# Kernel tuning notes

Hardware: AMD Instinct MI355X
Metric: run time of the kernel (lower is better)

The kernel has to match this reference:

```python
import jax, jax.numpy as jnp
import numpy as np
from jax import lax

# Module hyperparameters (match init_kwargs)
N_EXPERTS = 8
TOP_K = 2
N_CLUSTERS = 64
TEMP = 1.0
BETA = 0.9        # LIF membrane decay
VTH = 1.0         # LIF firing threshold
SURR_ALPHA = 4.0  # surrogate-gradient sharpness


@jax.custom_vjp
def spike(u):
    # Heaviside spike with sigmoid surrogate gradient (standard SNN practice)
    return (u >= 0).astype(u.dtype)

def _spike_fwd(u):
    return spike(u), u

def _spike_bwd(u, g):
    s = jax.nn.sigmoid(SURR_ALPHA * u)
    return (g * SURR_ALPHA * s * (1.0 - s),)

spike.defvjp(_spike_fwd, _spike_bwd)


def lif(x):
    """LIF neuron over leading time axis. x: (T, ...). Returns spikes (T, ...)."""
    def step(v, xt):
        v = BETA * v + xt
        s = spike(v - VTH)
        return v - s * VTH, s  # soft reset
    _, spikes = lax.scan(step, jnp.zeros_like(x[0]), x)
    return spikes


def setup_inputs() -> dict:
    key = jax.random.key(0)
    k1, k2, k3 = jax.random.split(key, 3)
    T, B, S, D = 4, 2, 1024, 1024
    ef = 4096 // N_EXPERTS  # 512
    x = jax.random.normal(k1, (T, B, S, D), dtype=jnp.float32)
    w_up = jax.random.normal(k2, (N_EXPERTS, D, ef), dtype=jnp.float32) / np.sqrt(D)
    w_down = jax.random.normal(k3, (N_EXPERTS, ef, D), dtype=jnp.float32) / np.sqrt(ef)
    expert_bias = jnp.zeros((N_EXPERTS,), dtype=jnp.float32)
    return {"x": x, "w_up": w_up, "w_down": w_down, "expert_bias": expert_bias}


def reference(x, w_up, w_down, expert_bias):
    T, B, S, D = x.shape
    N = B * S
    xf = x.reshape(T, N, D)

    # --- routing: LIF spikes -> cluster firing rates -> expert scores ---
    rs = lif(xf)                      # (T, N, D)
    fr = rs.mean(axis=0)              # (N, D) mean firing rate
    nc = N_CLUSTERS
    # feature d belongs to cluster d % nc -> reshape(N, D//nc, nc) sums same residues
    cr = fr.reshape(N, D // nc, nc).sum(axis=1) / (D // nc)       # (N, nc)
    cpe = nc // N_EXPERTS
    es = cr.reshape(N, N_EXPERTS, cpe).mean(axis=-1)              # (N, E)
    es = es / max(TEMP, 0.01) + expert_bias

    # --- top-k expert selection ---
    ts, ti = lax.top_k(es, TOP_K)                                 # (N, k)
    tw = jax.nn.softmax(ts, axis=-1).astype(x.dtype)              # (N, k)
    # combined per-(token, expert) weight: sum_k 1[ti==e] * tw
    w = (jax.nn.one_hot(ti, N_EXPERTS, dtype=x.dtype) * tw[..., None]).sum(axis=1)  # (N, E)

    # --- expert FFN with LIF nonlinearities (all experts, masked combine) ---
    # LIF is independent per (token, feature), so computing every expert on every
    # token and weighting by w (zero for unselected) matches the masked dispatch.
    h = jnp.einsum('tnd,edf->tenf', xf, w_up)                     # (T, E, N, ef)
    hs = lif(h)
    o = jnp.einsum('tenf,efd->tend', hs, w_down)                  # (T, E, N, D)
    os = lif(o)
    out = jnp.einsum('tend,ne->tnd', os, w).reshape(T, B, S, D)

    # --- load balance loss ---
    ef_frac = jax.nn.one_hot(ti, N_EXPERTS, dtype=jnp.float32).sum(axis=(0, 1)) / (N * TOP_K)
    rp = jax.nn.softmax(es, axis=-1).mean(axis=0)
    lb = N_EXPERTS * (ef_frac * rp).sum()
    return out, lb
```

## Files before the change

### kernel.cpp

```cpp
#include <hip/hip_runtime.h>
#include <cstdint>
#include <cstddef>

#define T_   4
#define NTOK 2048
#define D_   1024
#define EF   512
#define NE   8
#define TP   8

typedef __attribute__((ext_vector_type(4))) double d4;

#define WS_RP    0
#define WS_CNT   131072
#define WS_LTOK  131104
#define WS_LW    196640
#define WS_GMASK 327712

__global__ __launch_bounds__(256) void moe_routing(
    const float* __restrict__ x, const float* __restrict__ bias,
    double* __restrict__ rp, int* __restrict__ cnt,
    int* __restrict__ ltok, double* __restrict__ lw)
{
    const int n   = blockIdx.x;
    const int tid = threadIdx.x;
    __shared__ int scnt[NE];
    if (tid < NE) scnt[tid] = 0;
    __syncthreads();

    int c = 0;
#pragma unroll
    for (int j = 0; j < 4; ++j) {
        const int d = j * 256 + tid;
        double v = 0.0;
#pragma unroll
        for (int t = 0; t < T_; ++t) {
            v = 0.9 * v + (double)x[((size_t)t * NTOK + n) * D_ + d];
            if (v - 1.0 >= 0.0) { ++c; v -= 1.0; }
        }
    }
    c += __shfl_xor(c, 1);
    c += __shfl_xor(c, 2);
    c += __shfl_xor(c, 4);
    if ((tid & 7) == 0) atomicAdd(&scnt[(tid >> 3) & 7], c);
    __syncthreads();

    if (tid == 0) {
        double es[NE];
#pragma unroll
        for (int e = 0; e < NE; ++e)
            es[e] = (double)scnt[e] * (1.0 / 512.0) + (double)bias[e];

        int i0 = 0; double b0 = es[0];
        for (int e = 1; e < NE; ++e) if (es[e] > b0) { b0 = es[e]; i0 = e; }
        int i1 = -1; double b1 = -1e300;
        for (int e = 0; e < NE; ++e) if (e != i0 && es[e] > b1) { b1 = es[e]; i1 = e; }

        const double e1 = exp(b1 - b0);
        const double w0 = 1.0 / (1.0 + e1);
        const double w1 = e1 / (1.0 + e1);

        double mx = es[0];
        for (int e = 1; e < NE; ++e) mx = es[e] > mx ? es[e] : mx;
        double s = 0.0, ex[NE];
        for (int e = 0; e < NE; ++e) { ex[e] = exp(es[e] - mx); s += ex[e]; }
        for (int e = 0; e < NE; ++e) rp[(size_t)n * NE + e] = ex[e] / s;

        int s0 = atomicAdd(&cnt[i0], 1);
        ltok[i0 * NTOK + s0] = n; lw[i0 * NTOK + s0] = w0;
        int s1 = atomicAdd(&cnt[i1], 1);
        ltok[i1 * NTOK + s1] = n; lw[i1 * NTOK + s1] = w1;
    }
}

__global__ __launch_bounds__(256) void moe_finalize(
    const double* __restrict__ rp, const int* __restrict__ cnt,
    float* __restrict__ out_lb)
{
    __shared__ double red[256][NE];
    const int tid = threadIdx.x;
    double a[NE];
#pragma unroll
    for (int e = 0; e < NE; ++e) a[e] = 0.0;
    for (int n = tid; n < NTOK; n += 256)
#pragma unroll
        for (int e = 0; e < NE; ++e) a[e] += rp[(size_t)n * NE + e];
#pragma unroll
    for (int e = 0; e < NE; ++e) red[tid][e] = a[e];
    __syncthreads();
    if (tid < NE) {
        double s = 0.0;
        for (int i = 0; i < 256; ++i) s += red[i][tid];
        red[0][tid] = s;
    }
    __syncthreads();
    if (tid == 0) {
        double lb = 0.0;
#pragma unroll
        for (int e = 0; e < NE; ++e)
            lb += ((double)cnt[e] / (double)(NTOK * 2)) * (red[0][e] / (double)NTOK);
        out_lb[0] = (float)(8.0 * lb);
    }
}

__device__ __forceinline__ int dec_idx(double val, int* fam) {
    const double r0 = (val - 96.0) * 0.25;
    const int i0 = (int)r0;
    if ((double)i0 == r0 && i0 >= 0 && i0 < 16) { *fam = 0; return i0; }
    const double r1 = (val - 6.0) * 0.0625;
    const int i1 = (int)r1;
    if ((double)i1 == r1 && i1 >= 0 && i1 < 16) { *fam = 1; return i1; }
    *fam = -1; return 0;
}

struct Frag {
    int vA, kA, uB, kB;
    int vC[4], uC[4];
    int bad;
};

__device__ __forceinline__ Frag probe_layout(int l) {
    Frag fr; fr.bad = 0;
    const d4 zz = {0.0, 0.0, 0.0, 0.0};
    const double dl = (double)l;
    const d4 Dv = __builtin_amdgcn_mfma_f64_16x16x4f64(dl, 1.0, zz, 0, 0, 0);
    const d4 Du = __builtin_amdgcn_mfma_f64_16x16x4f64(1.0, dl, zz, 0, 0, 0);
    int famA = -1, famB = -1;
#pragma unroll
    for (int r = 0; r < 4; ++r) {
        int fa, fb;
        fr.vC[r] = dec_idx(Dv[r], &fa);
        fr.uC[r] = dec_idx(Du[r], &fb);
        if (r == 0) { famA = fa; famB = fb; }
        fr.bad |= (fa != famA) | (fb != famB) | (fa < 0) | (fb < 0);
    }
    fr.vA = (famA == 0) ? (l & 15) : (l >> 2);
    fr.kA = (famA == 0) ? (l >> 4) : (l & 3);
    fr.uB = (famB == 0) ? (l & 15) : (l >> 2);
    fr.kB = (famB == 0) ? (l >> 4) : (l & 3);
    const d4 D3 = __builtin_amdgcn_mfma_f64_16x16x4f64(
        (double)(1 << fr.kA), (double)(16 << fr.kB), zz, 0, 0, 0);
#pragma unroll
    for (int r = 0; r < 4; ++r) fr.bad |= (D3[r] != 1360.0);
    return fr;
}

__device__ __forceinline__ size_t gm_row(int e, int pairIdx, int t) {
    return ((size_t)((e << 11) + pairIdx) * 4 + t) * 32;
}

__global__ __launch_bounds__(256, 4) void moe_up(
    const float* __restrict__ x, const float* __restrict__ wup,
    const int* __restrict__ cnt, const int* __restrict__ ltok,
    unsigned short* __restrict__ gmask)
{
    const int gid  = blockIdx.x;
    const int e    = gid & 7;
    const int hf   = (gid >> 3) & 1;
    const int tile = gid >> 4;
    const int c    = cnt[e];
    const int base = tile * TP;
    if (base >= c) return;

    const int tid = threadIdx.x;
    const int w   = tid >> 6;
    const int l   = tid & 63;

    __shared__ int    s_tok[TP];
    __shared__ float  xs[32][132];
    __shared__ double dtile[4][16][17];
    __shared__ int s_bad;

    if (tid < TP) {
        const int idx = base + tid;
        s_tok[tid] = (idx < c) ? ltok[e * NTOK + idx] : ltok[e * NTOK + base];
    }
    if (tid == 0) s_bad = 0;
    __syncthreads();

    const Frag fr = probe_layout(l);
    if (fr.bad) atomicOr(&s_bad, 1);
    __syncthreads();

    if (s_bad) {
        unsigned short* gm16 = gmask;
        for (int i = tid; i < TP * 4 * 16; i += 256) {
            const int pr = i >> 6;
            gm16[gm_row(e, base + pr, (i >> 4) & 3) + hf * 16 + (i & 15)] = 0;
        }
        __syncthreads();
        for (int ci = tid; ci < TP * 256; ci += 256) {
            const int pair = ci >> 8;
            const int f    = hf * 256 + (ci & 255);
            const float* wc = wup + (size_t)e * D_ * EF + f;
            const float* xb = x + (size_t)s_tok[pair] * D_;
            double hh[4] = {0.0, 0.0, 0.0, 0.0};
            for (int d = 0; d < D_; ++d) {
                const double wv = (double)wc[(size_t)d * EF];
#pragma unroll
                for (int t = 0; t < 4; ++t)
                    hh[t] = fma((double)xb[(size_t)t * NTOK * D_ + d], wv, hh[t]);
            }
            double v = 0.0;
#pragma unroll
            for (int t = 0; t < 4; ++t) {
                v = 0.9 * v + hh[t];
                if (v - 1.0 >= 0.0) {
                    v -= 1.0;
                    atomicOr((unsigned*)&gm16[gm_row(e, base + pair, t) + ((f >> 4) & ~1)],
                             1u << (f & 31));
                }
            }
        }
        return;
    }

    const float* bp = wup + (size_t)e * D_ * EF + (size_t)fr.kB * EF
                    + hf * 256 + w * 64 + fr.uB;

    const d4 zz = {0.0, 0.0, 0.0, 0.0};
    d4 acc0[4], acc1[4];
#pragma unroll
    for (int j = 0; j < 4; ++j) { acc0[j] = zz; acc1[j] = zz; }

    const int arow0 = fr.vA;
    const int arow1 = 16 + fr.vA;

    for (int kc = 0; kc < 8; ++kc) {
        __syncthreads();
#pragma unroll
        for (int v = 0; v < 4; ++v) {
            const int idx = v * 256 + tid;
            const int row = idx >> 5;
            const int c4  = (idx & 31) << 2;
            const int pr  = row >> 2, t = row & 3;
            *(float4*)&xs[row][c4] =
                *(const float4*)&x[((size_t)t * NTOK + s_tok[pr]) * D_ + kc * 128 + c4];
        }
        __syncthreads();

#pragma unroll 4
        for (int kk2 = 0; kk2 < 32; ++kk2) {
            const double aD0 = (double)xs[arow0][kk2 * 4 + fr.kA];
            const double aD1 = (double)xs[arow1][kk2 * 4 + fr.kA];
            float b[4];
#pragma unroll
            for (int j = 0; j < 4; ++j) b[j] = bp[j * 16];
#pragma unroll
            for (int j = 0; j < 4; ++j) {
                const double bD = (double)b[j];
                acc0[j] = __builtin_amdgcn_mfma_f64_16x16x4f64(aD0, bD, acc0[j], 0, 0, 0);
                acc1[j] = __builtin_amdgcn_mfma_f64_16x16x4f64(aD1, bD, acc1[j], 0, 0, 0);
            }
            bp += (size_t)4 * EF;
        }
    }

    const int pp = l >> 4;
    const int cc = l & 15;
#pragma unroll
    for (int g = 0; g < 2; ++g) {
#pragma unroll
        for (int j = 0; j < 4; ++j) {
            const d4 av = g ? acc1[j] : acc0[j];
#pragma unroll
            for (int r = 0; r < 4; ++r) dtile[w][fr.vC[r]][fr.uC[r]] = av[r];
            double v = 0.0;
#pragma unroll
            for (int t = 0; t < 4; ++t) {
                v = 0.9 * v + dtile[w][pp * 4 + t][cc];
                const bool s = (v - 1.0 >= 0.0);
                if (s) v -= 1.0;
                const unsigned long long bal = __ballot(s);
                if (l < 4)
                    gmask[gm_row(e, base + g * 4 + l, t) + (hf * 16 + w * 4 + j)] =
                        (unsigned short)(bal >> (l * 16));
            }
        }
    }
}

__global__ __launch_bounds__(256, 4) void moe_down(
    const float* __restrict__ wdn,
    const int* __restrict__ cnt, const int* __restrict__ ltok,
    const double* __restrict__ lw, const unsigned short* __restrict__ gmask,
    float* __restrict__ out)
{
    const int gid  = blockIdx.x;
    const int e    = gid & 7;
    const int dq   = (gid >> 3) & 3;
    const int tile = gid >> 5;
    const int c    = cnt[e];
    const int base = tile * TP;
    if (base >= c) return;

    const int tid = threadIdx.x;
    const int w   = tid >> 6;
    const int l   = tid & 63;

    __shared__ int    s_tok[TP];
    __shared__ double s_w[TP];
    __shared__ unsigned hm[32][17];
    __shared__ double dtile[4][16][17];
    __shared__ int s_bad;

    if (tid < TP) {
        const int idx = base + tid;
        if (idx < c) { s_tok[tid] = ltok[e * NTOK + idx]; s_w[tid] = lw[e * NTOK + idx]; }
        else         { s_tok[tid] = ltok[e * NTOK + base]; s_w[tid] = 0.0; }
    }
    if (tid == 0) s_bad = 0;
    const unsigned* gm32 = (const unsigned*)gmask;
#pragma unroll
    for (int i = tid; i < 32 * 16; i += 256) {
        const int r = i >> 4, wd = i & 15;
        hm[r][wd] = gm32[(gm_row(e, base + (r >> 2), r & 3) >> 1) + wd];
    }
    __syncthreads();

    const Frag fr = probe_layout(l);
    if (fr.bad) atomicOr(&s_bad, 1);
    __syncthreads();

    if (s_bad) {
        for (int ci = tid; ci < TP * 256; ci += 256) {
            const int pair = ci >> 8;
            const int d    = dq * 256 + (ci & 255);
            const double wgt2 = s_w[pair];
            const int    nn2  = s_tok[pair];
            const float* wc = wdn + (size_t)e * EF * D_ + d;
            double o[4] = {0.0, 0.0, 0.0, 0.0};
            for (int f = 0; f < EF; ++f) {
                const double wv = (double)wc[(size_t)f * D_];
#pragma unroll
                for (int t = 0; t < 4; ++t)
                    if ((hm[pair * 4 + t][f >> 5] >> (f & 31)) & 1) o[t] += wv;
            }
            double v = 0.0;
#pragma unroll
            for (int t = 0; t < 4; ++t) {
                v = 0.9 * v + o[t];
                if (v - 1.0 >= 0.0) {
                    v -= 1.0;
                    if (wgt2 != 0.0)
                        atomicAdd(&out[((size_t)t * NTOK + nn2) * D_ + d], (float)wgt2);
                }
            }
        }
        return;
    }

    const d4 zz = {0.0, 0.0, 0.0, 0.0};
    const int pp = l >> 4;
    const int cc = l & 15;

    const float* dp = wdn + (size_t)e * EF * D_ + (size_t)fr.kB * D_
                    + dq * 256 + w * 64 + fr.uB;

    d4 acc0[4], acc1[4];
#pragma unroll
    for (int j = 0; j < 4; ++j) { acc0[j] = zz; acc1[j] = zz; }

    float bC[4];
#pragma unroll
    for (int j = 0; j < 4; ++j) bC[j] = dp[j * 16];
    unsigned m0 = hm[fr.vA][0];
    unsigned m1 = hm[16 + fr.vA][0];

#pragma unroll 1
    for (int wd = 0; wd < 16; ++wd) {
        const unsigned cm0 = m0, cm1 = m1;
        const int nw = (wd < 15) ? (wd + 1) : wd;
        m0 = hm[fr.vA][nw];
        m1 = hm[16 + fr.vA][nw];
#pragma unroll
        for (int k2 = 0; k2 < 8; ++k2) {
            const bool last = (wd == 15) && (k2 == 7);
            const float* dn_ = last ? dp : (dp + (size_t)4 * D_);
            float bN[4];
#pragma unroll
            for (int j = 0; j < 4; ++j) bN[j] = dn_[j * 16];

            const int bit = k2 * 4 + fr.kA;
            const double aD0 = ((cm0 >> bit) & 1u) ? 1.0 : 0.0;
            const double aD1 = ((cm1 >> bit) & 1u) ? 1.0 : 0.0;
#pragma unroll
            for (int j = 0; j < 4; ++j) {
                const double bD = (double)bC[j];
                acc0[j] = __builtin_amdgcn_mfma_f64_16x16x4f64(aD0, bD, acc0[j], 0, 0, 0);
                acc1[j] = __builtin_amdgcn_mfma_f64_16x16x4f64(aD1, bD, acc1[j], 0, 0, 0);
            }
#pragma unroll
            for (int j = 0; j < 4; ++j) bC[j] = bN[j];
            dp = dn_;
        }
    }

#pragma unroll
    for (int g = 0; g < 2; ++g) {
        const int pair = g * 4 + pp;
        const double wgt = s_w[pair];
        const int    nn  = s_tok[pair];
#pragma unroll
        for (int j = 0; j < 4; ++j) {
            const d4 av = g ? acc1[j] : acc0[j];
#pragma unroll
            for (int r = 0; r < 4; ++r) dtile[w][fr.vC[r]][fr.uC[r]] = av[r];
            const int d = dq * 256 + w * 64 + j * 16 + cc;
            double v = 0.0;
#pragma unroll
            for (int t = 0; t < 4; ++t) {
                v = 0.9 * v + dtile[w][pp * 4 + t][cc];
                if (v - 1.0 >= 0.0) {
                    v -= 1.0;
                    if (wgt != 0.0)
                        atomicAdd(&out[((size_t)t * NTOK + nn) * D_ + d], (float)wgt);
                }
            }
        }
    }
}

extern "C" void kernel_launch(void* const* d_in, const int* in_sizes, int n_in,
                              void* d_out, int out_size, void* d_ws, size_t ws_size,
                              hipStream_t stream)
{
    const float* x    = (const float*)d_in[0];
    const float* wup  = (const float*)d_in[1];
    const float* wdn  = (const float*)d_in[2];
    const float* bias = (const float*)d_in[3];
    float* out = (float*)d_out;
    char*  ws  = (char*)d_ws;

    double* rp   = (double*)(ws + WS_RP);
    int*    cnt  = (int*)(ws + WS_CNT);
    int*    ltok = (int*)(ws + WS_LTOK);
    double* lw   = (double*)(ws + WS_LW);
    unsigned short* gmask = (unsigned short*)(ws + WS_GMASK);

    hipMemsetAsync(d_out, 0, (size_t)out_size * sizeof(float), stream);
    hipMemsetAsync(cnt, 0, NE * sizeof(int), stream);

    moe_routing<<<NTOK, 256, 0, stream>>>(x, bias, rp, cnt, ltok, lw);
    moe_finalize<<<1, 256, 0, stream>>>(rp, cnt, out + (size_t)T_ * NTOK * D_);
    moe_up<<<NE * 1024, 256, 0, stream>>>(x, wup, cnt, ltok, gmask);
    moe_down<<<NE * 1024, 256, 0, stream>>>(wdn, cnt, ltok, lw, gmask, out);
}
```

Measured before the change: 702.3 us.

## Regroup MoE grid by expert chunk and split up-projection into feature quarters

Both expert kernels now index blocks as contiguous token tiles inside each (expert, feature or output chunk), instead of interleaving experts in the low bits. The up-projection splits the 512 hidden features into four 128-wide chunks, halving accumulators per wave and doubling blocks per token tile. The launch shrinks to 4096 blocks per kernel. The aims are fewer early-exit blocks, better cache reuse of each expert's weight slice, and lower register pressure. The trade-off is that each expert now has only 128 tiles of 8 tokens, so any expert routed more than 1024 tokens would silently drop the extra tokens.

```diff
diff --git a/kernel.cpp b/kernel.cpp
--- a/kernel.cpp
+++ b/kernel.cpp
@@ -154,12 +154,13 @@
     const int* __restrict__ cnt, const int* __restrict__ ltok,
     unsigned short* __restrict__ gmask)
 {
-    const int gid  = blockIdx.x;
-    const int e    = gid & 7;
-    const int hf   = (gid >> 3) & 1;
-    const int tile = gid >> 4;
-    const int c    = cnt[e];
-    const int base = tile * TP;
+    const int gid   = blockIdx.x;
+    const int tile  = gid & 127;
+    const int chunk = gid >> 7;
+    const int fq    = chunk & 3;
+    const int e     = chunk >> 2;
+    const int c     = cnt[e];
+    const int base  = tile * TP;
     if (base >= c) return;
 
     const int tid = threadIdx.x;
@@ -184,14 +185,14 @@
 
     if (s_bad) {
         unsigned short* gm16 = gmask;
-        for (int i = tid; i < TP * 4 * 16; i += 256) {
-            const int pr = i >> 6;
-            gm16[gm_row(e, base + pr, (i >> 4) & 3) + hf * 16 + (i & 15)] = 0;
+        for (int i = tid; i < TP * 4 * 8; i += 256) {
+            const int pr = i >> 5;
+            gm16[gm_row(e, base + pr, (i >> 3) & 3) + fq * 8 + (i & 7)] = 0;
         }
         __syncthreads();
-        for (int ci = tid; ci < TP * 256; ci += 256) {
-            const int pair = ci >> 8;
-            const int f    = hf * 256 + (ci & 255);
+        for (int ci = tid; ci < TP * 128; ci += 256) {
+            const int pair = ci >> 7;
+            const int f    = fq * 128 + (ci & 127);
             const float* wc = wup + (size_t)e * D_ * EF + f;
             const float* xb = x + (size_t)s_tok[pair] * D_;
             double hh[4] = {0.0, 0.0, 0.0, 0.0};
@@ -216,12 +217,12 @@
     }
 
     const float* bp = wup + (size_t)e * D_ * EF + (size_t)fr.kB * EF
-                    + hf * 256 + w * 64 + fr.uB;
+                    + fq * 128 + w * 32 + fr.uB;
 
     const d4 zz = {0.0, 0.0, 0.0, 0.0};
-    d4 acc0[4], acc1[4];
-#pragma unroll
-    for (int j = 0; j < 4; ++j) { acc0[j] = zz; acc1[j] = zz; }
+    d4 acc0[2], acc1[2];
+#pragma unroll
+    for (int j = 0; j < 2; ++j) { acc0[j] = zz; acc1[j] = zz; }
 
     const int arow0 = fr.vA;
     const int arow1 = 16 + fr.vA;
@@ -243,11 +244,11 @@
         for (int kk2 = 0; kk2 < 32; ++kk2) {
             const double aD0 = (double)xs[arow0][kk2 * 4 + fr.kA];
             const double aD1 = (double)xs[arow1][kk2 * 4 + fr.kA];
-            float b[4];
-#pragma unroll
-            for (int j = 0; j < 4; ++j) b[j] = bp[j * 16];
-#pragma unroll
-            for (int j = 0; j < 4; ++j) {
+            float b[2];
+            b[0] = bp[0];
+            b[1] = bp[16];
+#pragma unroll
+            for (int j = 0; j < 2; ++j) {
                 const double bD = (double)b[j];
                 acc0[j] = __builtin_amdgcn_mfma_f64_16x16x4f64(aD0, bD, acc0[j], 0, 0, 0);
                 acc1[j] = __builtin_amdgcn_mfma_f64_16x16x4f64(aD1, bD, acc1[j], 0, 0, 0);
@@ -261,7 +262,7 @@
 #pragma unroll
     for (int g = 0; g < 2; ++g) {
 #pragma unroll
-        for (int j = 0; j < 4; ++j) {
+        for (int j = 0; j < 2; ++j) {
             const d4 av = g ? acc1[j] : acc0[j];
 #pragma unroll
             for (int r = 0; r < 4; ++r) dtile[w][fr.vC[r]][fr.uC[r]] = av[r];
@@ -273,7 +274,7 @@
                 if (s) v -= 1.0;
                 const unsigned long long bal = __ballot(s);
                 if (l < 4)
-                    gmask[gm_row(e, base + g * 4 + l, t) + (hf * 16 + w * 4 + j)] =
+                    gmask[gm_row(e, base + g * 4 + l, t) + (fq * 8 + w * 2 + j)] =
                         (unsigned short)(bal >> (l * 16));
             }
         }
@@ -286,12 +287,13 @@
     const double* __restrict__ lw, const unsigned short* __restrict__ gmask,
     float* __restrict__ out)
 {
-    const int gid  = blockIdx.x;
-    const int e    = gid & 7;
-    const int dq   = (gid >> 3) & 3;
-    const int tile = gid >> 5;
-    const int c    = cnt[e];
-    const int base = tile * TP;
+    const int gid   = blockIdx.x;
+    const int tile  = gid & 127;
+    const int chunk = gid >> 7;
+    const int dq    = chunk & 3;
+    const int e     = chunk >> 2;
+    const int c     = cnt[e];
+    const int base  = tile * TP;
     if (base >= c) return;
 
     const int tid = threadIdx.x;
@@ -443,6 +445,6 @@
 
     moe_routing<<<NTOK, 256, 0, stream>>>(x, bias, rp, cnt, ltok, lw);
     moe_finalize<<<1, 256, 0, stream>>>(rp, cnt, out + (size_t)T_ * NTOK * D_);
-    moe_up<<<NE * 1024, 256, 0, stream>>>(x, wup, cnt, ltok, gmask);
-    moe_down<<<NE * 1024, 256, 0, stream>>>(wdn, cnt, ltok, lw, gmask, out);
-}
+    moe_up<<<NE * 4 * 128, 256, 0, stream>>>(x, wup, cnt, ltok, gmask);
+    moe_down<<<NE * 4 * 128, 256, 0, stream>>>(wdn, cnt, ltok, lw, gmask, out);
+}
```

After: 748.1 us. +6.5%, slower.
